# Kernel optimization log

Measured on AMD Instinct MI355X. Metric: run time of the kernel, lower is better.

The kernel has to match this reference:

```python
import jax, jax.numpy as jnp
import numpy as np

S, B, F, U = 8, 65536, 256, 256  # N_species, N_batch, N_feats, N_units (depth=2)


def setup_inputs() -> dict:
    key = jax.random.key(0)
    ks = jax.random.split(key, 9)
    b = jax.random.normal(ks[0], (S, B, F), dtype=jnp.float32)
    # Per-species weights stacked along species axis (equivalent to ModuleList of Linears).
    # nn.Linear default init: U(-1/sqrt(fan_in), 1/sqrt(fan_in)) -- exact dist doesn't matter
    # for a correctness baseline; scale similarly.
    def lin(k, fan_in, shape):
        lim = 1.0 / np.sqrt(fan_in)
        return jax.random.uniform(k, shape, dtype=jnp.float32, minval=-lim, maxval=lim)
    W1 = lin(ks[1], F, (S, F, U)); b1 = lin(ks[2], F, (S, U))
    W2 = lin(ks[3], U, (S, U, U)); b2 = lin(ks[4], U, (S, U))
    W3 = lin(ks[5], U, (S, U, U)); b3 = lin(ks[6], U, (S, U))
    W4 = lin(ks[7], U, (S, U, 1)); b4 = lin(ks[8], U, (S, 1))
    return {"b": b, "W1": W1, "b1": b1, "W2": W2, "b2": b2,
            "W3": W3, "b3": b3, "W4": W4, "b4": b4}


def _leaky(x):
    return jnp.where(x >= 0, x, 0.1 * x)  # LeakyReLU(0.1)


def reference(b, W1, b1, W2, b2, W3, b3, W4, b4):
    # depth == 2 path. Dropout(p=0.01) is identity in eval mode.
    # Per-species batched GEMMs: (S,B,in) x (S,in,out) -> (S,B,out)
    x = _leaky(jnp.einsum('sbf,sfu->sbu', b, W1) + b1[:, None, :])
    x = _leaky(jnp.einsum('sbu,suv->sbv', x, W2) + b2[:, None, :])
    x = _leaky(jnp.einsum('sbu,suv->sbv', x, W3) + b3[:, None, :])
    A = jnp.einsum('sbu,suo->sbo', x, W4) + b4[:, None, :]  # (S, B, 1)
    return jax.nn.sigmoid(A.sum(axis=0))  # (B, 1)
```

## Files before the change

kernel.cpp:

```cpp
#include <hip/hip_runtime.h>

typedef __bf16 bf16x8 __attribute__((ext_vector_type(8)));
typedef float  f32x4  __attribute__((ext_vector_type(4)));
typedef float  fvec4  __attribute__((ext_vector_type(4)));

#define NSPEC 8
#define NB    65536
#define NF    256

__global__ __launch_bounds__(256) void wconv_kernel(
    const float* __restrict__ W1, const float* __restrict__ W2,
    const float* __restrict__ W3, __bf16* __restrict__ WT)
{
    __shared__ float tile[32][33];
    int bid = blockIdx.x;
    int l   = bid >> 9;
    int rem = bid & 511;
    int s   = rem >> 6;
    int tt  = rem & 63;
    int ti  = tt >> 3, tj = tt & 7;
    const float* W   = (l == 0) ? W1 : (l == 1) ? W2 : W3;
    const float* ibs = W + (size_t)s * 65536;
    int c  = threadIdx.x & 31;
    int r0 = threadIdx.x >> 5;
#pragma unroll
    for (int k = 0; k < 4; ++k) {
        int r = r0 + k * 8;
        tile[r][c] = ibs[(ti * 32 + r) * 256 + tj * 32 + c];
    }
    __syncthreads();
    __bf16* obs = WT + ((size_t)(l * 8 + s)) * 65536;
#pragma unroll
    for (int k = 0; k < 4; ++k) {
        int r = r0 + k * 8;
        obs[(tj * 32 + r) * 256 + ti * 32 + c] = (__bf16)tile[c][r];
    }
}

#define GLLD(gp, lp)                                                     \
    __builtin_amdgcn_global_load_lds(                                    \
        (const __attribute__((address_space(1))) char*)(gp),             \
        (__attribute__((address_space(3))) char*)(lp), 16, 0, 0)

#define BAR()                                                            \
    do {                                                                 \
        __builtin_amdgcn_sched_barrier(0);                               \
        asm volatile("s_waitcnt lgkmcnt(0)" ::: "memory");               \
        __builtin_amdgcn_s_barrier();                                    \
        __builtin_amdgcn_sched_barrier(0);                               \
    } while (0)

__global__ __launch_bounds__(256, 2) void mlp_kernel(
    const float* __restrict__ bIn, const float* __restrict__ b1,
    const float* __restrict__ b2,  const float* __restrict__ b3,
    const float* __restrict__ W4,  const float* __restrict__ b4,
    const __bf16* __restrict__ WT, float* __restrict__ P)
{
    __shared__ __align__(16) __bf16 act[64 * 256];
    __shared__ __align__(16) char  wlds[3][16384];

    const int t    = threadIdx.x;
    const int lane = t & 63;
    const int wave = t >> 6;
    const int l15  = lane & 15;
    const int g    = lane >> 4;
    const int wv   = wave * 64;
    const int s    = blockIdx.x & 7;
    const int row0 = (blockIdx.x >> 3) * 64;
    const int swzB = l15 << 4;
    char* const pA = (char*)act;

    int gll_off[4];
#pragma unroll
    for (int i = 0; i < 4; ++i) {
        int v = wv + i * 16 + (lane >> 2);
        int q = (lane & 3) ^ ((v >> 1) & 3);
        gll_off[i] = v * 512 + q * 16;
    }

    const char* const wt0 = (const char*)(WT + ((size_t)(0 * 8 + s) << 16));
    const char* const wt1 = (const char*)(WT + ((size_t)(1 * 8 + s) << 16));
    const char* const wt2 = (const char*)(WT + ((size_t)(2 * 8 + s) << 16));

#define ISSUE_CHUNK(wtb, gci)                                            \
    do {                                                                 \
        char* lp0 = (char*)&wlds[(gci) % 3][wave * 4096];                \
        GLLD((wtb) + gll_off[0] + ((gci) & 7) * 64, lp0);                \
        GLLD((wtb) + gll_off[1] + ((gci) & 7) * 64, lp0 + 1024);         \
        GLLD((wtb) + gll_off[2] + ((gci) & 7) * 64, lp0 + 2048);         \
        GLLD((wtb) + gll_off[3] + ((gci) & 7) * 64, lp0 + 3072);         \
    } while (0)

#define READ_SET(AF, BF, gci, kslice)                                    \
    do {                                                                 \
        const char* wbuf_ = (const char*)wlds[(gci) % 3];                \
        _Pragma("unroll")                                                \
        for (int m_ = 0; m_ < 4; ++m_) {                                 \
            int row_ = wv + m_ * 16 + l15;                               \
            AF[m_] = *(const bf16x8*)(wbuf_ + row_ * 64 +                \
                                      ((g ^ ((row_ >> 1) & 3)) << 4));   \
        }                                                                \
        _Pragma("unroll")                                                \
        for (int n_ = 0; n_ < 4; ++n_)                                   \
            BF[n_] = *(const bf16x8*)(pA + (n_ * 16 + l15) * 512 +       \
                                      (((kslice) * 64 + g * 16) ^ swzB));\
    } while (0)

#define MFMA_SET(AF, BF)                                                 \
    do {                                                                 \
        __builtin_amdgcn_s_setprio(1);                                   \
        _Pragma("unroll")                                                \
        for (int m_ = 0; m_ < 4; ++m_)                                   \
            _Pragma("unroll")                                            \
            for (int n_ = 0; n_ < 4; ++n_)                               \
                acc[m_][n_] = __builtin_amdgcn_mfma_f32_16x16x32_bf16(   \
                    AF[m_], BF[n_], acc[m_][n_], 0, 0, 0);               \
        __builtin_amdgcn_s_setprio(0);                                   \
    } while (0)

    fvec4 bias[3][4];
#pragma unroll
    for (int l = 0; l < 3; ++l) {
        const float* bl = (l == 0 ? b1 : l == 1 ? b2 : b3) + s * 256;
#pragma unroll
        for (int m = 0; m < 4; ++m)
            bias[l][m] = *(const fvec4*)(bl + wv + m * 16 + g * 4);
    }

    const float* src = bIn + ((size_t)s * NB + row0) * NF;
#pragma unroll
    for (int it = 0; it < 16; ++it) {
        int flat = it * 1024 + t * 4;
        int r = flat >> 8;
        int f = flat & 255;
        fvec4 v = __builtin_nontemporal_load((const fvec4*)(src + flat));
        union { __bf16 h[4]; unsigned long long q; } pk;
        pk.h[0] = (__bf16)v[0]; pk.h[1] = (__bf16)v[1];
        pk.h[2] = (__bf16)v[2]; pk.h[3] = (__bf16)v[3];
        *(unsigned long long*)(pA + r * 512 + ((f * 2) ^ ((r & 15) << 4))) = pk.q;
    }

    ISSUE_CHUNK(wt0, 0);
    ISSUE_CHUNK(wt0, 1);
    ISSUE_CHUNK(wt0, 2);
    BAR();

#pragma unroll
    for (int l = 0; l < 3; ++l) {
        const int c0 = l * 8;
        f32x4 acc[4][4];
#pragma unroll
        for (int m = 0; m < 4; ++m)
#pragma unroll
            for (int n = 0; n < 4; ++n)
                acc[m][n] = (f32x4){0.f, 0.f, 0.f, 0.f};

        bf16x8 afX[4], bfX[4], afY[4], bfY[4];
        asm volatile("s_waitcnt vmcnt(8)" ::: "memory");
        READ_SET(afX, bfX, c0, 0);

#pragma unroll
        for (int ks = 0; ks < 8; ++ks) {
            const int c = c0 + ks;
            if (ks < 7) {
                if (c <= 21) asm volatile("s_waitcnt vmcnt(4)" ::: "memory");
                else         asm volatile("s_waitcnt vmcnt(0)" ::: "memory");
                if ((ks & 1) == 0) READ_SET(afY, bfY, c + 1, ks + 1);
                else               READ_SET(afX, bfX, c + 1, ks + 1);
                asm volatile("s_waitcnt lgkmcnt(8)" ::: "memory");
            } else {
                asm volatile("s_waitcnt lgkmcnt(0)" ::: "memory");
            }
            const int gci = c + 3;
            if (gci <= 23) {
                const char* wtc = (gci < 8) ? wt0 : (gci < 16) ? wt1 : wt2;
                ISSUE_CHUNK(wtc, gci);
            }
            __builtin_amdgcn_sched_barrier(0);
            if ((ks & 1) == 0) MFMA_SET(afX, bfX);
            else               MFMA_SET(afY, bfY);
            __builtin_amdgcn_sched_barrier(0);
        }

        BAR();

#pragma unroll
        for (int m = 0; m < 4; ++m) {
            int vbyte = (wv + m * 16 + g * 4) * 2;
#pragma unroll
            for (int n = 0; n < 4; ++n) {
                union { __bf16 h[4]; unsigned long long q; } pk;
#pragma unroll
                for (int j = 0; j < 4; ++j) {
                    float x = acc[m][n][j] + bias[l][m][j];
                    x = (x >= 0.f) ? x : 0.1f * x;
                    pk.h[j] = (__bf16)x;
                }
                *(unsigned long long*)(pA + (n * 16 + l15) * 512 + (vbyte ^ swzB)) = pk.q;
            }
        }
        BAR();
    }

    const int r4   = t >> 2;
    const int u0   = (t & 3) * 64;
    const int swz4 = (r4 & 15) << 4;
    const float* w4s = W4 + s * 256 + u0;
    float part = 0.f;
#pragma unroll
    for (int i = 0; i < 8; ++i) {
        bf16x8 x = *(const bf16x8*)(pA + r4 * 512 + (((u0 + i * 8) * 2) ^ swz4));
        fvec4 wlo = *(const fvec4*)(w4s + i * 8);
        fvec4 whi = *(const fvec4*)(w4s + i * 8 + 4);
        part += (float)x[0] * wlo[0] + (float)x[1] * wlo[1] +
                (float)x[2] * wlo[2] + (float)x[3] * wlo[3] +
                (float)x[4] * whi[0] + (float)x[5] * whi[1] +
                (float)x[6] * whi[2] + (float)x[7] * whi[3];
    }
    part += __shfl_xor(part, 1);
    part += __shfl_xor(part, 2);
    if ((t & 3) == 0) P[(size_t)s * NB + row0 + r4] = part + b4[s];
}

__global__ __launch_bounds__(256) void reduce_kernel(
    const float* __restrict__ P, float* __restrict__ out)
{
    int i = blockIdx.x * 256 + threadIdx.x;
    float a = 0.f;
#pragma unroll
    for (int sp = 0; sp < NSPEC; ++sp) a += P[(size_t)sp * NB + i];
    out[i] = 1.f / (1.f + __expf(-a));
}

extern "C" void kernel_launch(void* const* d_in, const int* in_sizes, int n_in,
                              void* d_out, int out_size, void* d_ws, size_t ws_size,
                              hipStream_t stream)
{
    const float* bIn = (const float*)d_in[0];
    const float* W1  = (const float*)d_in[1];
    const float* b1  = (const float*)d_in[2];
    const float* W2  = (const float*)d_in[3];
    const float* b2  = (const float*)d_in[4];
    const float* W3  = (const float*)d_in[5];
    const float* b3  = (const float*)d_in[6];
    const float* W4  = (const float*)d_in[7];
    const float* b4  = (const float*)d_in[8];
    __bf16* WT = (__bf16*)d_ws;
    float*  P  = (float*)((char*)d_ws + (3u << 20));

    wconv_kernel<<<1536, 256, 0, stream>>>(W1, W2, W3, WT);
    mlp_kernel<<<8192, 256, 0, stream>>>(bIn, b1, b2, b3, W4, b4, WT, P);
    reduce_kernel<<<NB / 256, 256, 0, stream>>>(P, (float*)d_out);
}
```

Measured before the change: 324.8 us.

## Make MLP kernel persistent with per-wave full weight planes and input prefetch

Turns the MLP kernel into a persistent kernel: 256 blocks each loop over 32 row tiles instead of launching one block per tile. Each wave now keeps a full 8-slot weight plane in LDS. The next layer's weights are streamed into a slot as soon as that slot is consumed, and the next tile's input rows are loaded into registers during the last layer. This is meant to hide weight and input load latency and to drop per-block setup cost. In exchange, LDS use grows, occupancy falls to one block per CU, and the hand-tuned vmcnt waits get more complex.

```diff
diff --git a/kernel.cpp b/kernel.cpp
--- a/kernel.cpp
+++ b/kernel.cpp
@@ -7,6 +7,7 @@
 #define NSPEC 8
 #define NB    65536
 #define NF    256
+#define NITEMS 32
 
 __global__ __launch_bounds__(256) void wconv_kernel(
     const float* __restrict__ W1, const float* __restrict__ W2,
@@ -50,14 +51,14 @@
         __builtin_amdgcn_sched_barrier(0);                               \
     } while (0)
 
-__global__ __launch_bounds__(256, 2) void mlp_kernel(
+__global__ __launch_bounds__(256, 1) void mlp_kernel(
     const float* __restrict__ bIn, const float* __restrict__ b1,
     const float* __restrict__ b2,  const float* __restrict__ b3,
     const float* __restrict__ W4,  const float* __restrict__ b4,
     const __bf16* __restrict__ WT, float* __restrict__ P)
 {
     __shared__ __align__(16) __bf16 act[64 * 256];
-    __shared__ __align__(16) char  wlds[3][16384];
+    __shared__ __align__(16) char  wpl[4][8][4096];
 
     const int t    = threadIdx.x;
     const int lane = t & 63;
@@ -66,9 +67,10 @@
     const int g    = lane >> 4;
     const int wv   = wave * 64;
     const int s    = blockIdx.x & 7;
-    const int row0 = (blockIdx.x >> 3) * 64;
+    const int tile0 = (blockIdx.x >> 3) * NITEMS;
     const int swzB = l15 << 4;
     char* const pA = (char*)act;
+    char* const plane = (char*)wpl + wave * 32768;
 
     int gll_off[4];
 #pragma unroll
@@ -82,22 +84,22 @@
     const char* const wt1 = (const char*)(WT + ((size_t)(1 * 8 + s) << 16));
     const char* const wt2 = (const char*)(WT + ((size_t)(2 * 8 + s) << 16));
 
-#define ISSUE_CHUNK(wtb, gci)                                            \
-    do {                                                                 \
-        char* lp0 = (char*)&wlds[(gci) % 3][wave * 4096];                \
-        GLLD((wtb) + gll_off[0] + ((gci) & 7) * 64, lp0);                \
-        GLLD((wtb) + gll_off[1] + ((gci) & 7) * 64, lp0 + 1024);         \
-        GLLD((wtb) + gll_off[2] + ((gci) & 7) * 64, lp0 + 2048);         \
-        GLLD((wtb) + gll_off[3] + ((gci) & 7) * 64, lp0 + 3072);         \
-    } while (0)
-
-#define READ_SET(AF, BF, gci, kslice)                                    \
-    do {                                                                 \
-        const char* wbuf_ = (const char*)wlds[(gci) % 3];                \
+#define ISSUE_P(wtb, ks)                                                 \
+    do {                                                                 \
+        char* lp0 = plane + (ks) * 4096;                                 \
+        GLLD((wtb) + gll_off[0] + (ks) * 64, lp0);                       \
+        GLLD((wtb) + gll_off[1] + (ks) * 64, lp0 + 1024);                \
+        GLLD((wtb) + gll_off[2] + (ks) * 64, lp0 + 2048);                \
+        GLLD((wtb) + gll_off[3] + (ks) * 64, lp0 + 3072);                \
+    } while (0)
+
+#define READP(AF, BF, slot, kslice)                                      \
+    do {                                                                 \
+        const char* pb_ = plane + (slot) * 4096;                         \
         _Pragma("unroll")                                                \
         for (int m_ = 0; m_ < 4; ++m_) {                                 \
             int row_ = wv + m_ * 16 + l15;                               \
-            AF[m_] = *(const bf16x8*)(wbuf_ + row_ * 64 +                \
+            AF[m_] = *(const bf16x8*)(pb_ + (m_ * 16 + l15) * 64 +       \
                                       ((g ^ ((row_ >> 1) & 3)) << 4));   \
         }                                                                \
         _Pragma("unroll")                                                \
@@ -126,100 +128,127 @@
         for (int m = 0; m < 4; ++m)
             bias[l][m] = *(const fvec4*)(bl + wv + m * 16 + g * 4);
     }
-
-    const float* src = bIn + ((size_t)s * NB + row0) * NF;
-#pragma unroll
-    for (int it = 0; it < 16; ++it) {
-        int flat = it * 1024 + t * 4;
-        int r = flat >> 8;
-        int f = flat & 255;
-        fvec4 v = __builtin_nontemporal_load((const fvec4*)(src + flat));
-        union { __bf16 h[4]; unsigned long long q; } pk;
-        pk.h[0] = (__bf16)v[0]; pk.h[1] = (__bf16)v[1];
-        pk.h[2] = (__bf16)v[2]; pk.h[3] = (__bf16)v[3];
-        *(unsigned long long*)(pA + r * 512 + ((f * 2) ^ ((r & 15) << 4))) = pk.q;
-    }
-
-    ISSUE_CHUNK(wt0, 0);
-    ISSUE_CHUNK(wt0, 1);
-    ISSUE_CHUNK(wt0, 2);
-    BAR();
-
-#pragma unroll
-    for (int l = 0; l < 3; ++l) {
-        const int c0 = l * 8;
-        f32x4 acc[4][4];
-#pragma unroll
-        for (int m = 0; m < 4; ++m)
-#pragma unroll
-            for (int n = 0; n < 4; ++n)
-                acc[m][n] = (f32x4){0.f, 0.f, 0.f, 0.f};
-
-        bf16x8 afX[4], bfX[4], afY[4], bfY[4];
-        asm volatile("s_waitcnt vmcnt(8)" ::: "memory");
-        READ_SET(afX, bfX, c0, 0);
-
-#pragma unroll
-        for (int ks = 0; ks < 8; ++ks) {
-            const int c = c0 + ks;
-            if (ks < 7) {
-                if (c <= 21) asm volatile("s_waitcnt vmcnt(4)" ::: "memory");
-                else         asm volatile("s_waitcnt vmcnt(0)" ::: "memory");
-                if ((ks & 1) == 0) READ_SET(afY, bfY, c + 1, ks + 1);
-                else               READ_SET(afX, bfX, c + 1, ks + 1);
-                asm volatile("s_waitcnt lgkmcnt(8)" ::: "memory");
-            } else {
-                asm volatile("s_waitcnt lgkmcnt(0)" ::: "memory");
-            }
-            const int gci = c + 3;
-            if (gci <= 23) {
-                const char* wtc = (gci < 8) ? wt0 : (gci < 16) ? wt1 : wt2;
-                ISSUE_CHUNK(wtc, gci);
-            }
-            __builtin_amdgcn_sched_barrier(0);
-            if ((ks & 1) == 0) MFMA_SET(afX, bfX);
-            else               MFMA_SET(afY, bfY);
-            __builtin_amdgcn_sched_barrier(0);
-        }
-
-        BAR();
-
-#pragma unroll
-        for (int m = 0; m < 4; ++m) {
-            int vbyte = (wv + m * 16 + g * 4) * 2;
-#pragma unroll
-            for (int n = 0; n < 4; ++n) {
-                union { __bf16 h[4]; unsigned long long q; } pk;
-#pragma unroll
-                for (int j = 0; j < 4; ++j) {
-                    float x = acc[m][n][j] + bias[l][m][j];
-                    x = (x >= 0.f) ? x : 0.1f * x;
-                    pk.h[j] = (__bf16)x;
-                }
-                *(unsigned long long*)(pA + (n * 16 + l15) * 512 + (vbyte ^ swzB)) = pk.q;
-            }
-        }
-        BAR();
-    }
-
     const int r4   = t >> 2;
     const int u0   = (t & 3) * 64;
     const int swz4 = (r4 & 15) << 4;
     const float* w4s = W4 + s * 256 + u0;
-    float part = 0.f;
-#pragma unroll
-    for (int i = 0; i < 8; ++i) {
-        bf16x8 x = *(const bf16x8*)(pA + r4 * 512 + (((u0 + i * 8) * 2) ^ swz4));
-        fvec4 wlo = *(const fvec4*)(w4s + i * 8);
-        fvec4 whi = *(const fvec4*)(w4s + i * 8 + 4);
-        part += (float)x[0] * wlo[0] + (float)x[1] * wlo[1] +
-                (float)x[2] * wlo[2] + (float)x[3] * wlo[3] +
-                (float)x[4] * whi[0] + (float)x[5] * whi[1] +
-                (float)x[6] * whi[2] + (float)x[7] * whi[3];
-    }
-    part += __shfl_xor(part, 1);
-    part += __shfl_xor(part, 2);
-    if ((t & 3) == 0) P[(size_t)s * NB + row0 + r4] = part + b4[s];
+    const float  b4s = b4[s];
+
+    {
+        const float* src = bIn + ((size_t)s * NB + (size_t)tile0 * 64) * NF;
+#pragma unroll
+        for (int it = 0; it < 16; ++it) {
+            int flat = it * 1024 + t * 4;
+            int r = flat >> 8;
+            int f = flat & 255;
+            fvec4 v = __builtin_nontemporal_load((const fvec4*)(src + flat));
+            union { __bf16 h[4]; unsigned long long q; } pk;
+            pk.h[0] = (__bf16)v[0]; pk.h[1] = (__bf16)v[1];
+            pk.h[2] = (__bf16)v[2]; pk.h[3] = (__bf16)v[3];
+            *(unsigned long long*)(pA + r * 512 + ((f * 2) ^ ((r & 15) << 4))) = pk.q;
+        }
+    }
+#pragma unroll
+    for (int ks = 0; ks < 8; ++ks) ISSUE_P(wt0, ks);
+    BAR();
+
+    for (int item = 0; item < NITEMS; ++item) {
+        const int row0 = (tile0 + item) * 64;
+        const bool last = (item == NITEMS - 1);
+        fvec4 stg[16];
+
+#pragma unroll
+        for (int L = 0; L < 3; ++L) {
+            const char* wtn = (L == 0) ? wt1 : (L == 1) ? wt2 : wt0;
+            const bool fetch = (L < 2) || !last;
+
+            f32x4 acc[4][4];
+#pragma unroll
+            for (int m = 0; m < 4; ++m)
+#pragma unroll
+                for (int n = 0; n < 4; ++n)
+                    acc[m][n] = (f32x4){0.f, 0.f, 0.f, 0.f};
+
+            bf16x8 afX[4], bfX[4], afY[4], bfY[4];
+            asm volatile("s_waitcnt vmcnt(28)" ::: "memory");
+            READP(afX, bfX, 0, 0);
+
+#pragma unroll
+            for (int ks = 0; ks < 8; ++ks) {
+                if (ks < 7) {
+                    asm volatile("s_waitcnt vmcnt(24)" ::: "memory");
+                    if ((ks & 1) == 0) READP(afY, bfY, ks + 1, ks + 1);
+                    else               READP(afX, bfX, ks + 1, ks + 1);
+                    asm volatile("s_waitcnt lgkmcnt(8)" ::: "memory");
+                } else {
+                    asm volatile("s_waitcnt lgkmcnt(0)" ::: "memory");
+                }
+                __builtin_amdgcn_sched_barrier(0);
+                if (fetch) ISSUE_P(wtn, ks);
+                __builtin_amdgcn_sched_barrier(0);
+                if ((ks & 1) == 0) MFMA_SET(afX, bfX);
+                else               MFMA_SET(afY, bfY);
+                __builtin_amdgcn_sched_barrier(0);
+            }
+
+            if (L == 2 && !last) {
+                const float* src = bIn + ((size_t)s * NB + (size_t)(row0 + 64)) * NF;
+#pragma unroll
+                for (int it = 0; it < 16; ++it)
+                    stg[it] = __builtin_nontemporal_load((const fvec4*)(src + it * 1024 + t * 4));
+            }
+
+            BAR();
+
+#pragma unroll
+            for (int m = 0; m < 4; ++m) {
+                int vbyte = (wv + m * 16 + g * 4) * 2;
+#pragma unroll
+                for (int n = 0; n < 4; ++n) {
+                    union { __bf16 h[4]; unsigned long long q; } pk;
+#pragma unroll
+                    for (int j = 0; j < 4; ++j) {
+                        float x = acc[m][n][j] + bias[L][m][j];
+                        x = (x >= 0.f) ? x : 0.1f * x;
+                        pk.h[j] = (__bf16)x;
+                    }
+                    *(unsigned long long*)(pA + (n * 16 + l15) * 512 + (vbyte ^ swzB)) = pk.q;
+                }
+            }
+            BAR();
+        }
+
+        float part = 0.f;
+#pragma unroll
+        for (int i = 0; i < 8; ++i) {
+            bf16x8 x = *(const bf16x8*)(pA + r4 * 512 + (((u0 + i * 8) * 2) ^ swz4));
+            fvec4 wlo = *(const fvec4*)(w4s + i * 8);
+            fvec4 whi = *(const fvec4*)(w4s + i * 8 + 4);
+            part += (float)x[0] * wlo[0] + (float)x[1] * wlo[1] +
+                    (float)x[2] * wlo[2] + (float)x[3] * wlo[3] +
+                    (float)x[4] * whi[0] + (float)x[5] * whi[1] +
+                    (float)x[6] * whi[2] + (float)x[7] * whi[3];
+        }
+        part += __shfl_xor(part, 1);
+        part += __shfl_xor(part, 2);
+        if ((t & 3) == 0) P[(size_t)s * NB + row0 + r4] = part + b4s;
+
+        if (!last) {
+            asm volatile("s_waitcnt vmcnt(1)" ::: "memory");
+            BAR();
+#pragma unroll
+            for (int it = 0; it < 16; ++it) {
+                int flat = it * 1024 + t * 4;
+                int r = flat >> 8;
+                int f = flat & 255;
+                union { __bf16 h[4]; unsigned long long q; } pk;
+                pk.h[0] = (__bf16)stg[it][0]; pk.h[1] = (__bf16)stg[it][1];
+                pk.h[2] = (__bf16)stg[it][2]; pk.h[3] = (__bf16)stg[it][3];
+                *(unsigned long long*)(pA + r * 512 + ((f * 2) ^ ((r & 15) << 4))) = pk.q;
+            }
+            BAR();
+        }
+    }
 }
 
 __global__ __launch_bounds__(256) void reduce_kernel(
@@ -249,6 +278,6 @@
     float*  P  = (float*)((char*)d_ws + (3u << 20));
 
     wconv_kernel<<<1536, 256, 0, stream>>>(W1, W2, W3, WT);
-    mlp_kernel<<<8192, 256, 0, stream>>>(bIn, b1, b2, b3, W4, b4, WT, P);
+    mlp_kernel<<<256, 256, 0, stream>>>(bIn, b1, b2, b3, W4, b4, WT, P);
     reduce_kernel<<<NB / 256, 256, 0, stream>>>(P, (float*)d_out);
 }
```

Result: slower. 419.2 us (+29.1%).

## Double batch rows per block and give each wave a 128x64 output tile

Applied to the files above, without the earlier changes.

Each block now processes 128 batch rows instead of 64, and the four waves form a 2x2 grid of 128-unit by 64-row tiles, each with its own private triple-buffered weight plane in LDS. Each wave issues eight MFMAs per B fragment, which raises arithmetic intensity per LDS read and halves how often weights are reloaded per batch row. In exchange it doubles accumulator registers, limits occupancy to one block per CU because LDS use grows, and halves the grid. Wait counts and the final W4 dot-product reduction are adjusted to match.

```diff
diff --git a/kernel.cpp b/kernel.cpp
--- a/kernel.cpp
+++ b/kernel.cpp
@@ -50,59 +50,58 @@
         __builtin_amdgcn_sched_barrier(0);                               \
     } while (0)
 
-__global__ __launch_bounds__(256, 2) void mlp_kernel(
+__global__ __launch_bounds__(256, 1) void mlp_kernel(
     const float* __restrict__ bIn, const float* __restrict__ b1,
     const float* __restrict__ b2,  const float* __restrict__ b3,
     const float* __restrict__ W4,  const float* __restrict__ b4,
     const __bf16* __restrict__ WT, float* __restrict__ P)
 {
-    __shared__ __align__(16) __bf16 act[64 * 256];
-    __shared__ __align__(16) char  wlds[3][16384];
+    __shared__ __align__(16) __bf16 act[128 * 256];
+    __shared__ __align__(16) char  wpl[4][3][8192];
 
     const int t    = threadIdx.x;
     const int lane = t & 63;
     const int wave = t >> 6;
     const int l15  = lane & 15;
     const int g    = lane >> 4;
-    const int wv   = wave * 64;
+    const int wv   = (wave & 1) * 128;
+    const int bb   = (wave >> 1) * 64;
     const int s    = blockIdx.x & 7;
-    const int row0 = (blockIdx.x >> 3) * 64;
+    const int row0 = (blockIdx.x >> 3) * 128;
     const int swzB = l15 << 4;
     char* const pA = (char*)act;
-
-    int gll_off[4];
-#pragma unroll
-    for (int i = 0; i < 4; ++i) {
-        int v = wv + i * 16 + (lane >> 2);
-        int q = (lane & 3) ^ ((v >> 1) & 3);
-        gll_off[i] = v * 512 + q * 16;
+    char* const plane0 = (char*)wpl[wave];
+
+    int gll_off[8];
+#pragma unroll
+    for (int i = 0; i < 8; ++i) {
+        int rl = i * 16 + (lane >> 2);
+        int q  = (lane & 3) ^ ((rl >> 1) & 3);
+        gll_off[i] = (wv + rl) * 512 + q * 16;
     }
 
     const char* const wt0 = (const char*)(WT + ((size_t)(0 * 8 + s) << 16));
     const char* const wt1 = (const char*)(WT + ((size_t)(1 * 8 + s) << 16));
     const char* const wt2 = (const char*)(WT + ((size_t)(2 * 8 + s) << 16));
 
-#define ISSUE_CHUNK(wtb, gci)                                            \
-    do {                                                                 \
-        char* lp0 = (char*)&wlds[(gci) % 3][wave * 4096];                \
-        GLLD((wtb) + gll_off[0] + ((gci) & 7) * 64, lp0);                \
-        GLLD((wtb) + gll_off[1] + ((gci) & 7) * 64, lp0 + 1024);         \
-        GLLD((wtb) + gll_off[2] + ((gci) & 7) * 64, lp0 + 2048);         \
-        GLLD((wtb) + gll_off[3] + ((gci) & 7) * 64, lp0 + 3072);         \
-    } while (0)
-
-#define READ_SET(AF, BF, gci, kslice)                                    \
-    do {                                                                 \
-        const char* wbuf_ = (const char*)wlds[(gci) % 3];                \
-        _Pragma("unroll")                                                \
-        for (int m_ = 0; m_ < 4; ++m_) {                                 \
-            int row_ = wv + m_ * 16 + l15;                               \
-            AF[m_] = *(const bf16x8*)(wbuf_ + row_ * 64 +                \
-                                      ((g ^ ((row_ >> 1) & 3)) << 4));   \
-        }                                                                \
+#define ISSUE_CHUNK(wtb, c)                                              \
+    do {                                                                 \
+        char* lp_ = plane0 + ((c) % 3) * 8192;                           \
+        _Pragma("unroll")                                                \
+        for (int i_ = 0; i_ < 8; ++i_)                                   \
+            GLLD((wtb) + gll_off[i_] + ((c) & 7) * 64, lp_ + i_ * 1024); \
+    } while (0)
+
+#define READ_SET(AF, BF, c, kslice)                                      \
+    do {                                                                 \
+        const char* pb_ = plane0 + ((c) % 3) * 8192;                     \
+        _Pragma("unroll")                                                \
+        for (int m_ = 0; m_ < 8; ++m_)                                   \
+            AF[m_] = *(const bf16x8*)(pb_ + (m_ * 16 + l15) * 64 +       \
+                                      ((g ^ ((l15 >> 1) & 3)) << 4));    \
         _Pragma("unroll")                                                \
         for (int n_ = 0; n_ < 4; ++n_)                                   \
-            BF[n_] = *(const bf16x8*)(pA + (n_ * 16 + l15) * 512 +       \
+            BF[n_] = *(const bf16x8*)(pA + (bb + n_ * 16 + l15) * 512 +  \
                                       (((kslice) * 64 + g * 16) ^ swzB));\
     } while (0)
 
@@ -110,7 +109,7 @@
     do {                                                                 \
         __builtin_amdgcn_s_setprio(1);                                   \
         _Pragma("unroll")                                                \
-        for (int m_ = 0; m_ < 4; ++m_)                                   \
+        for (int m_ = 0; m_ < 8; ++m_)                                   \
             _Pragma("unroll")                                            \
             for (int n_ = 0; n_ < 4; ++n_)                               \
                 acc[m_][n_] = __builtin_amdgcn_mfma_f32_16x16x32_bf16(   \
@@ -118,18 +117,18 @@
         __builtin_amdgcn_s_setprio(0);                                   \
     } while (0)
 
-    fvec4 bias[3][4];
+    fvec4 bias[3][8];
 #pragma unroll
     for (int l = 0; l < 3; ++l) {
         const float* bl = (l == 0 ? b1 : l == 1 ? b2 : b3) + s * 256;
 #pragma unroll
-        for (int m = 0; m < 4; ++m)
+        for (int m = 0; m < 8; ++m)
             bias[l][m] = *(const fvec4*)(bl + wv + m * 16 + g * 4);
     }
 
     const float* src = bIn + ((size_t)s * NB + row0) * NF;
 #pragma unroll
-    for (int it = 0; it < 16; ++it) {
+    for (int it = 0; it < 32; ++it) {
         int flat = it * 1024 + t * 4;
         int r = flat >> 8;
         int f = flat & 255;
@@ -140,6 +139,12 @@
         *(unsigned long long*)(pA + r * 512 + ((f * 2) ^ ((r & 15) << 4))) = pk.q;
     }
 
+#pragma unroll
+    for (int l = 0; l < 3; ++l)
+#pragma unroll
+        for (int m = 0; m < 8; ++m)
+            asm volatile("" :: "v"(bias[l][m]));
+
     ISSUE_CHUNK(wt0, 0);
     ISSUE_CHUNK(wt0, 1);
     ISSUE_CHUNK(wt0, 2);
@@ -148,26 +153,26 @@
 #pragma unroll
     for (int l = 0; l < 3; ++l) {
         const int c0 = l * 8;
-        f32x4 acc[4][4];
-#pragma unroll
-        for (int m = 0; m < 4; ++m)
+        f32x4 acc[8][4];
+#pragma unroll
+        for (int m = 0; m < 8; ++m)
 #pragma unroll
             for (int n = 0; n < 4; ++n)
                 acc[m][n] = (f32x4){0.f, 0.f, 0.f, 0.f};
 
-        bf16x8 afX[4], bfX[4], afY[4], bfY[4];
-        asm volatile("s_waitcnt vmcnt(8)" ::: "memory");
+        bf16x8 afX[8], bfX[4], afY[8], bfY[4];
+        asm volatile("s_waitcnt vmcnt(16)" ::: "memory");
         READ_SET(afX, bfX, c0, 0);
 
 #pragma unroll
         for (int ks = 0; ks < 8; ++ks) {
             const int c = c0 + ks;
             if (ks < 7) {
-                if (c <= 21) asm volatile("s_waitcnt vmcnt(4)" ::: "memory");
+                if (c <= 21) asm volatile("s_waitcnt vmcnt(8)" ::: "memory");
                 else         asm volatile("s_waitcnt vmcnt(0)" ::: "memory");
                 if ((ks & 1) == 0) READ_SET(afY, bfY, c + 1, ks + 1);
                 else               READ_SET(afX, bfX, c + 1, ks + 1);
-                asm volatile("s_waitcnt lgkmcnt(8)" ::: "memory");
+                asm volatile("s_waitcnt lgkmcnt(12)" ::: "memory");
             } else {
                 asm volatile("s_waitcnt lgkmcnt(0)" ::: "memory");
             }
@@ -185,7 +190,7 @@
         BAR();
 
 #pragma unroll
-        for (int m = 0; m < 4; ++m) {
+        for (int m = 0; m < 8; ++m) {
             int vbyte = (wv + m * 16 + g * 4) * 2;
 #pragma unroll
             for (int n = 0; n < 4; ++n) {
@@ -196,19 +201,19 @@
                     x = (x >= 0.f) ? x : 0.1f * x;
                     pk.h[j] = (__bf16)x;
                 }
-                *(unsigned long long*)(pA + (n * 16 + l15) * 512 + (vbyte ^ swzB)) = pk.q;
+                *(unsigned long long*)(pA + (bb + n * 16 + l15) * 512 + (vbyte ^ swzB)) = pk.q;
             }
         }
         BAR();
     }
 
-    const int r4   = t >> 2;
-    const int u0   = (t & 3) * 64;
+    const int r4   = t >> 1;
+    const int u0   = (t & 1) * 128;
     const int swz4 = (r4 & 15) << 4;
     const float* w4s = W4 + s * 256 + u0;
     float part = 0.f;
 #pragma unroll
-    for (int i = 0; i < 8; ++i) {
+    for (int i = 0; i < 16; ++i) {
         bf16x8 x = *(const bf16x8*)(pA + r4 * 512 + (((u0 + i * 8) * 2) ^ swz4));
         fvec4 wlo = *(const fvec4*)(w4s + i * 8);
         fvec4 whi = *(const fvec4*)(w4s + i * 8 + 4);
@@ -218,8 +223,7 @@
                 (float)x[6] * whi[2] + (float)x[7] * whi[3];
     }
     part += __shfl_xor(part, 1);
-    part += __shfl_xor(part, 2);
-    if ((t & 3) == 0) P[(size_t)s * NB + row0 + r4] = part + b4[s];
+    if ((t & 1) == 0) P[(size_t)s * NB + row0 + r4] = part + b4[s];
 }
 
 __global__ __launch_bounds__(256) void reduce_kernel(
@@ -249,6 +253,6 @@
     float*  P  = (float*)((char*)d_ws + (3u << 20));
 
     wconv_kernel<<<1536, 256, 0, stream>>>(W1, W2, W3, WT);
-    mlp_kernel<<<8192, 256, 0, stream>>>(bIn, b1, b2, b3, W4, b4, WT, P);
+    mlp_kernel<<<4096, 256, 0, stream>>>(bIn, b1, b2, b3, W4, b4, WT, P);
     reduce_kernel<<<NB / 256, 256, 0, stream>>>(P, (float*)d_out);
 }
```

Measured after the change: 329.5 us. About the same (+1.4%).
